# Performance work log

Measured on AMD Instinct MI355X. Metric: run time of the kernel, lower is better.

Reference implementation:

```python
import jax, jax.numpy as jnp
import numpy as np

COST_CLASS = 1.0
COST_OBJECTNESS = 5.0
COST_GIOU = 2.0
COST_CENTER = 10.0

B, Q, G, C = 32, 1024, 64, 256


def _lsa(cost):
    """Exact rectangular linear sum assignment (Jonker-Volgenant shortest
    augmenting path, same algorithm as scipy.optimize.linear_sum_assignment).
    cost: (R, Cc) float64 numpy array. Returns (row_ind, col_ind), row_ind sorted."""
    transposed = cost.shape[0] > cost.shape[1]
    if transposed:
        cost = cost.T
    n, m = cost.shape
    u = np.zeros(n)
    v = np.zeros(m)
    col4row = np.full(n, -1, dtype=np.int64)
    row4col = np.full(m, -1, dtype=np.int64)
    for cur_row in range(n):
        shortest = np.full(m, np.inf)
        path = np.full(m, -1, dtype=np.int64)
        SC = np.zeros(m, dtype=bool)
        SR_rows = []
        min_val = 0.0
        i = cur_row
        sink = -1
        while sink == -1:
            SR_rows.append(i)
            idx = np.where(~SC)[0]
            r = min_val + cost[i, idx] - u[i] - v[idx]
            better = r < shortest[idx]
            upd = idx[better]
            shortest[upd] = r[better]
            path[upd] = i
            j = idx[np.argmin(shortest[idx])]
            min_val = shortest[j]
            SC[j] = True
            if row4col[j] == -1:
                sink = j
            else:
                i = row4col[j]
        # dual variable update
        u[cur_row] += min_val
        for irow in SR_rows:
            if irow != cur_row:
                u[irow] += min_val - shortest[col4row[irow]]
        v[SC] -= min_val - shortest[SC]
        # augment along the alternating path back to cur_row
        j = sink
        while True:
            i = path[j]
            row4col[j] = i
            col4row[i], j = j, col4row[i]
            if i == cur_row:
                break
    if transposed:
        order = np.argsort(col4row)
        return col4row[order], np.arange(n)[order]
    return np.arange(n), col4row


def setup_inputs() -> dict:
    key = jax.random.key(0)
    k1, k2, k3, k4, k5 = jax.random.split(key, 5)
    return {
        "sem_cls_prob": jax.random.uniform(k1, (B, Q, C), dtype=jnp.float32),
        "objectness_prob": jax.random.uniform(k2, (B, Q), dtype=jnp.float32),
        "center_dist": jax.random.uniform(k3, (B, Q, G), dtype=jnp.float32),
        "gious": jax.random.uniform(k4, (B, Q, G), dtype=jnp.float32),
        "nactual_gt": jax.random.randint(k5, (B,), 0, G, dtype=jnp.int64)
        if jax.config.jax_enable_x64 else jax.random.randint(k5, (B,), 0, G).astype(jnp.int32),
    }


def reference(sem_cls_prob, objectness_prob, center_dist, gious, nactual_gt):
    batchsize, nprop = objectness_prob.shape
    # class_mat == 0 in the original module
    final_cost = (COST_OBJECTNESS * (-objectness_prob[..., None])
                  + COST_CENTER * center_dist
                  + COST_GIOU * (-gious))  # [B, Q, G]
    cost_np = np.asarray(final_cost, dtype=np.float64)
    ngt = np.asarray(nactual_gt)
    per_prop_gt_inds = np.zeros((batchsize, nprop), dtype=np.int64)
    proposal_matched_mask = np.zeros((batchsize, nprop), dtype=np.float32)
    for b in range(batchsize):  # per-batch independent Hungarian (as in source)
        g = int(ngt[b])
        if g > 0:
            rows, cols = _lsa(cost_np[b, :, :g])
            per_prop_gt_inds[b, rows] = cols
            proposal_matched_mask[b, rows] = 1.0
    return jnp.asarray(per_prop_gt_inds), jnp.asarray(proposal_matched_mask)
```

## Files before the change

kernel.cpp:

```cpp
#include <hip/hip_runtime.h>
#include <math.h>

#define B_ 32
#define Q_ 1024
#define G_ 64
#define K16 16

typedef double v16d __attribute__((ext_vector_type(16)));
typedef float  v16f __attribute__((ext_vector_type(16)));
typedef int    v16i __attribute__((ext_vector_type(16)));

#define REP16(OP) OP(0,0) OP(1,1) OP(2,2) OP(3,3) OP(4,4) OP(5,5) OP(6,6) OP(7,7) \
                  OP(8,8) OP(9,9) OP(10,a) OP(11,b) OP(12,c) OP(13,d) OP(14,e) OP(15,f)
#define REP16A(OP,A) OP(A,0,0) OP(A,1,1) OP(A,2,2) OP(A,3,3) OP(A,4,4) OP(A,5,5) OP(A,6,6) OP(A,7,7) \
                     OP(A,8,8) OP(A,9,9) OP(A,10,a) OP(A,11,b) OP(A,12,c) OP(A,13,d) OP(A,14,e) OP(A,15,f)

#define ROR1 0x121
#define ROR2 0x122
#define ROR4 0x124
#define ROR8 0x128
#define BC15 0x142
#define BC31 0x143

template<int CTRL>
__device__ __forceinline__ double dpp_f64(double x) {
    union { double d; int i[2]; } a; a.d = x;
    union { int i[2]; double d; } r;
    r.i[0] = __builtin_amdgcn_update_dpp(a.i[0], a.i[0], CTRL, 0xF, 0xF, false);
    r.i[1] = __builtin_amdgcn_update_dpp(a.i[1], a.i[1], CTRL, 0xF, 0xF, false);
    return r.d;
}
template<int CTRL>
__device__ __forceinline__ int dpp_i32(int x) {
    return __builtin_amdgcn_update_dpp(x, x, CTRL, 0xF, 0xF, false);
}

__device__ __forceinline__ double readlane_f64(double x, int sl) {
    const int s = __builtin_amdgcn_readfirstlane(sl);
    union { double d; int i2[2]; } a; a.d = x;
    union { int i2[2]; double d; } r;
    r.i2[0] = __builtin_amdgcn_readlane(a.i2[0], s);
    r.i2[1] = __builtin_amdgcn_readlane(a.i2[1], s);
    return r.d;
}
__device__ __forceinline__ double readlane_f64c(double x, int sl) {
    union { double d; int i2[2]; } a; a.d = x;
    union { int i2[2]; double d; } r;
    r.i2[0] = __builtin_amdgcn_readlane(a.i2[0], sl);
    r.i2[1] = __builtin_amdgcn_readlane(a.i2[1], sl);
    return r.d;
}
__device__ __forceinline__ float readlane_f32u(float x, int sl) {
    union { float f; int i; } a; a.f = x;
    union { int i; float f; } r;
    r.i = __builtin_amdgcn_readlane(a.i, __builtin_amdgcn_readfirstlane(sl));
    return r.f;
}
__device__ __forceinline__ int readlane_i32(int x, int sl) {
    return __builtin_amdgcn_readlane(x, __builtin_amdgcn_readfirstlane(sl));
}
__device__ __forceinline__ int readlane_i32c(int x, int sl) {
    return __builtin_amdgcn_readlane(x, sl);
}

__device__ __forceinline__ int sel16v_i(v16i p, int s) {
    const int t0_0 = (s & 1) ? p.s1 : p.s0;
    const int t0_1 = (s & 1) ? p.s3 : p.s2;
    const int t0_2 = (s & 1) ? p.s5 : p.s4;
    const int t0_3 = (s & 1) ? p.s7 : p.s6;
    const int t0_4 = (s & 1) ? p.s9 : p.s8;
    const int t0_5 = (s & 1) ? p.sb : p.sa;
    const int t0_6 = (s & 1) ? p.sd : p.sc;
    const int t0_7 = (s & 1) ? p.sf : p.se;
    const int t1_0 = (s & 2) ? t0_1 : t0_0;
    const int t1_1 = (s & 2) ? t0_3 : t0_2;
    const int t1_2 = (s & 2) ? t0_5 : t0_4;
    const int t1_3 = (s & 2) ? t0_7 : t0_6;
    const int a0 = (s & 4) ? t1_1 : t1_0;
    const int a1 = (s & 4) ? t1_3 : t1_2;
    return (s & 8) ? a1 : a0;
}
__device__ __forceinline__ double sel16v_d(v16d p, int s) {
    const double t0_0 = (s & 1) ? p.s1 : p.s0;
    const double t0_1 = (s & 1) ? p.s3 : p.s2;
    const double t0_2 = (s & 1) ? p.s5 : p.s4;
    const double t0_3 = (s & 1) ? p.s7 : p.s6;
    const double t0_4 = (s & 1) ? p.s9 : p.s8;
    const double t0_5 = (s & 1) ? p.sb : p.sa;
    const double t0_6 = (s & 1) ? p.sd : p.sc;
    const double t0_7 = (s & 1) ? p.sf : p.se;
    const double t1_0 = (s & 2) ? t0_1 : t0_0;
    const double t1_1 = (s & 2) ? t0_3 : t0_2;
    const double t1_2 = (s & 2) ? t0_5 : t0_4;
    const double t1_3 = (s & 2) ? t0_7 : t0_6;
    const double a0 = (s & 4) ? t1_1 : t1_0;
    const double a1 = (s & 4) ? t1_3 : t1_2;
    return (s & 8) ? a1 : a0;
}

__device__ __forceinline__ void lexpair(v16d c, int l,
                                        double& gv_o, int& jm_o) {
    const double a0 = fmin(c.s0, c.s1), a1 = fmin(c.s2, c.s3),
                 a2 = fmin(c.s4, c.s5), a3 = fmin(c.s6, c.s7),
                 a4 = fmin(c.s8, c.s9), a5 = fmin(c.sa, c.sb),
                 a6 = fmin(c.sc, c.sd), a7 = fmin(c.se, c.sf);
    const double b0 = fmin(a0, a1), b1 = fmin(a2, a3),
                 b2 = fmin(a4, a5), b3 = fmin(a6, a7);
    const double d0 = fmin(b0, b1), d1 = fmin(b2, b3);
    const double vloc = fmin(d0, d1);
    double v = vloc;
#define VS_(C) { const double pv = dpp_f64<C>(v); v = fmin(pv, v); }
    VS_(ROR1) VS_(ROR2) VS_(ROR4) VS_(ROR8) VS_(BC15) VS_(BC31)
#undef VS_
    const double gv = readlane_f64c(v, 63);
    const int bit3 = (d0 == gv) ? 0 : 1;
    const double bsel = bit3 ? b2 : b0;
    const int bit2 = (bsel == gv) ? 0 : 1;
    const double asel = bit2 ? (bit3 ? a6 : a2) : (bit3 ? a4 : a0);
    const int bit1 = (asel == gv) ? 0 : 1;
    const double csel = bit1 ? (bit2 ? (bit3 ? c.se : c.s6) : (bit3 ? c.sa : c.s2))
                             : (bit2 ? (bit3 ? c.sc : c.s4) : (bit3 ? c.s8 : c.s0));
    const int bit0 = (csel == gv) ? 0 : 1;
    const int kloc = (bit3 << 3) | (bit2 << 2) | (bit1 << 1) | bit0;
    int key = (vloc == gv) ? ((kloc << 6) | l) : 0x7FFFFFFF;
#define KS_(C) { const int pk = dpp_i32<C>(key); key = (pk < key) ? pk : key; }
    KS_(ROR1) KS_(ROR2) KS_(ROR4) KS_(ROR8) KS_(BC15) KS_(BC31)
#undef KS_
    jm_o = readlane_i32c(key, 63);
    gv_o = gv;
}

__global__ __launch_bounds__(256) void build_kernel(
    const float* __restrict__ obj, const float* __restrict__ cd,
    const float* __restrict__ gi, float* __restrict__ ct,
    float* __restrict__ pv, int* __restrict__ pj,
    float* __restrict__ pv2, int* __restrict__ pj2)
{
    __shared__ float tile[64][65];
    const int b  = blockIdx.y;
    const int jb = blockIdx.x << 6;
    const int t  = threadIdx.x;
    const float* objb = obj + (b << 10);
    const float4* cd4 = (const float4*)(cd + ((size_t)b << 16));
    const float4* gi4 = (const float4*)(gi + ((size_t)b << 16));

    #pragma unroll
    for (int p = 0; p < 4; ++p) {
        const int f  = t + (p << 8);
        const int jj = f >> 4;
        const int q  = f & 15;
        const int i0 = q << 2;
        const int j  = jb + jj;
        const float om = __fmul_rn(5.0f, -objb[j]);
        const float4 c4 = cd4[(j << 4) + q];
        const float4 q4 = gi4[(j << 4) + q];
        tile[i0 + 0][jj] = __fadd_rn(__fadd_rn(om, __fmul_rn(10.0f, c4.x)), __fmul_rn(2.0f, -q4.x));
        tile[i0 + 1][jj] = __fadd_rn(__fadd_rn(om, __fmul_rn(10.0f, c4.y)), __fmul_rn(2.0f, -q4.y));
        tile[i0 + 2][jj] = __fadd_rn(__fadd_rn(om, __fmul_rn(10.0f, c4.z)), __fmul_rn(2.0f, -q4.z));
        tile[i0 + 3][jj] = __fadd_rn(__fadd_rn(om, __fmul_rn(10.0f, c4.w)), __fmul_rn(2.0f, -q4.w));
    }
    __syncthreads();
    #pragma unroll
    for (int r = 0; r < 16; ++r) {
        const int idx = (r << 8) + t;
        const int i = idx >> 6, j2 = idx & 63;
        ct[(((size_t)(b << 6) + i) << 10) + jb + j2] = tile[i][j2];
    }
    if (t < 64) {
        float bv = tile[t][0]; int bc = 0;
        float sv = 1e30f;      int sc2 = 0;
        #pragma unroll 8
        for (int c = 1; c < 64; ++c) {
            const float v = tile[t][c];
            const bool t1 = v < bv;
            const bool t2 = (!t1) && (v < sv);
            sv  = t1 ? bv : (t2 ? v : sv);
            sc2 = t1 ? bc : (t2 ? c : sc2);
            bv  = t1 ? v : bv;
            bc  = t1 ? c : bc;
        }
        const int o = (((b << 6) + t) << 4) + blockIdx.x;
        pv[o]  = bv;  pj[o]  = jb + bc;
        pv2[o] = sv;  pj2[o] = jb + sc2;
    }
}

#define LD_W_(D,K,H) D.s##H = rp_[(K) << 6];
#define LD_N_(D,K,H) { const int idx_ = ((l + ((K) << 6)) << 6) + ri_; \
    D.s##H = __fadd_rn(__fadd_rn(objm.s##H, __fmul_rn(10.0f, cdb[idx_])), \
                       __fmul_rn(2.0f, -gib[idx_])); }
#define LOAD_ROW(ri, dst) { const int ri_ = (ri); \
    if (HASWS) { const float* rp_ = ctb + ((size_t)ri_ << 10) + l; REP16A(LD_W_, dst) } \
    else       { REP16A(LD_N_, dst) } }

template<bool HASWS>
__global__ __launch_bounds__(64, 1) void matcher_k(
    const float* __restrict__ obj, const float* __restrict__ cd,
    const float* __restrict__ gi, const int* __restrict__ ngt,
    const float* __restrict__ ct, const float* __restrict__ pv,
    const int* __restrict__ pj, const float* __restrict__ pv2,
    const int* __restrict__ pj2, float* __restrict__ out_ind,
    float* __restrict__ out_mask)
{
    const int b = blockIdx.x;
    const int l = threadIdx.x;
    const int g = ngt[b];

    const float* objb = obj + (b << 10);
    const float* cdb  = cd + ((size_t)b << 16);
    const float* gib  = gi + ((size_t)b << 16);
    const float* ctb  = HASWS ? (ct + ((size_t)(b << 6) << 10)) : (const float*)nullptr;

    v16f objm;
    if (!HASWS) {
#define OBJI_(K,H) objm.s##H = __fmul_rn(5.0f, -objb[l + (K << 6)]);
        REP16(OBJI_)
#undef OBJI_
    }

    float pre_v = 0.0f, sec_v = 0.0f; int pre_j = 0, sec_j = 0;
    if (HASWS) {
        const int base = ((b << 6) + l) << 4;
        const float4* pvq = (const float4*)(pv  + base);
        const int4*   pjq = (const int4*)(pj  + base);
        const float4* svq = (const float4*)(pv2 + base);
        const int4*   sjq = (const int4*)(pj2 + base);
        const float4 pA = pvq[0], pB = pvq[1], pC = pvq[2], pD = pvq[3];
        const int4   jA = pjq[0], jB = pjq[1], jC = pjq[2], jD = pjq[3];
        const float4 sA = svq[0], sB = svq[1], sC = svq[2], sD = svq[3];
        const int4   tA = sjq[0], tB = sjq[1], tC = sjq[2], tD = sjq[3];
        float bv = pA.x; int bj = jA.x; float sv = sA.x; int sj = tA.x;
#define MERGE_(CV,CJ,C2V,C2J) { const bool nb = (CV) < bv; \
    const bool s1 = (C2V) < bv; const bool s2 = (CV) < sv; \
    const float nsv = nb ? (s1 ? (C2V) : bv) : (s2 ? (CV) : sv); \
    const int   nsj = nb ? (s1 ? (C2J) : bj) : (s2 ? (CJ) : sj); \
    bj = nb ? (CJ) : bj; bv = nb ? (CV) : bv; sv = nsv; sj = nsj; }
        MERGE_(pA.y,jA.y,sA.y,tA.y) MERGE_(pA.z,jA.z,sA.z,tA.z) MERGE_(pA.w,jA.w,sA.w,tA.w)
        MERGE_(pB.x,jB.x,sB.x,tB.x) MERGE_(pB.y,jB.y,sB.y,tB.y) MERGE_(pB.z,jB.z,sB.z,tB.z) MERGE_(pB.w,jB.w,sB.w,tB.w)
        MERGE_(pC.x,jC.x,sC.x,tC.x) MERGE_(pC.y,jC.y,sC.y,tC.y) MERGE_(pC.z,jC.z,sC.z,tC.z) MERGE_(pC.w,jC.w,sC.w,tC.w)
        MERGE_(pD.x,jD.x,sD.x,tD.x) MERGE_(pD.y,jD.y,sD.y,tD.y) MERGE_(pD.z,jD.z,sD.z,tD.z) MERGE_(pD.w,jD.w,sD.w,tD.w)
#undef MERGE_
        pre_v = bv; pre_j = bj; sec_v = sv; sec_j = sj;
    } else if (g > 0) {
        for (int i = 0; i < g; ++i) {
            v16f c; LOAD_ROW(i, c)
            v16d c64;
#define CV_(K,H) c64.s##H = (double)c.s##H;
            REP16(CV_)
#undef CV_
            double gv; int j0;
            lexpair(c64, l, gv, j0);
            pre_v = (l == i) ? (float)gv : pre_v;
            pre_j = (l == i) ? j0 : pre_j;
        }
        sec_v = pre_v; sec_j = pre_j;
    }

    const double INF = __builtin_inf();
    double u_rep = 0.0;
    double m_rec = 0.0;
    bool   inSR  = false;
    int    c4r_rep = -1;
    unsigned asg   = 0u;
    unsigned dirty = 0u;
    v16d v_r, sh_r;
    v16i path;
    v16f c_cur, c_i;
#define INI_(K,H) { v_r.s##H = 0.0; sh_r.s##H = 0.0; path.s##H = 0; }
    REP16(INI_)
#undef INI_

    for (int cur = 0; cur < g; ++cur) {
        const float pre_vc = readlane_f32u(pre_v, cur);
        int jm = readlane_i32(pre_j, cur);
        double minv = (double)pre_vc;
        bool have_cur = false;
        {
            const int ow1 = jm & 63, sl1 = jm >> 6;
            const unsigned d1 = (unsigned)readlane_i32((int)dirty, ow1);
            if ((d1 >> sl1) & 1u) {
                const float sv_c = readlane_f32u(sec_v, cur);
                const int   sj_c = readlane_i32(sec_j, cur);
                const unsigned d2 = (unsigned)readlane_i32((int)dirty, sj_c & 63);
                if (!((d2 >> (sj_c >> 6)) & 1u)) {
                    const double vpj = readlane_f64(sel16v_d(v_r, sl1), ow1);
                    const double vA = (double)pre_vc - vpj;
                    const double vB = (double)sv_c;
                    const bool t = (vB < vA) || ((vB == vA) && (sj_c < jm));
                    minv = t ? vB : vA;
                    jm   = t ? sj_c : jm;
                } else {
                    LOAD_ROW(cur, c_cur) have_cur = true;
                    v16d rr0;
#define RR0_(K,H) rr0.s##H = (double)c_cur.s##H - v_r.s##H;
                    REP16(RR0_)
#undef RR0_
                    lexpair(rr0, l, minv, jm);
                }
            }
        }
        const unsigned long long mk0 = __ballot(c4r_rep == jm);

        if (mk0 == 0ull) {
            u_rep   = (l == cur) ? u_rep + minv : u_rep;
            c4r_rep = (l == cur) ? jm           : c4r_rep;
            asg     = (l == (jm & 63)) ? (asg | (1u << (jm >> 6))) : asg;
        } else {
            if (!have_cur) LOAD_ROW(cur, c_cur)
            int i = (int)__builtin_ctzll(mk0);
            LOAD_ROW(i, c_i)
            double ui = readlane_f64(u_rep, i);
            unsigned sc = (l == (jm & 63)) ? (1u << (jm >> 6)) : 0u;
            inSR  = (l == i);
            m_rec = minv;
#define SH0_(K,H) { sh_r.s##H = (double)c_cur.s##H - v_r.s##H; path.s##H = cur; }
            REP16(SH0_)
#undef SH0_

            int sink = -1;
            while (sink < 0) {
                v16d cand;
#define DST_(K,H) { const double rr = ((minv + (double)c_i.s##H) - ui) - v_r.s##H; \
                    const bool notSC = !((sc >> K) & 1u); \
                    const bool upd = notSC && (rr < sh_r.s##H);  \
                    sh_r.s##H = upd ? rr : sh_r.s##H; \
                    path.s##H = upd ? i : path.s##H; \
                    cand.s##H = notSC ? sh_r.s##H : INF; }
                REP16(DST_)
#undef DST_
                lexpair(cand, l, minv, jm);
                const unsigned long long mk = __ballot(c4r_rep == jm);
                if (l == (jm & 63)) sc |= (1u << (jm >> 6));
                if (mk == 0ull) {
                    sink = jm;
                } else {
                    i = (int)__builtin_ctzll(mk);
                    LOAD_ROW(i, c_i)
                    if (l == i) { inSR = true; m_rec = minv; }
                    ui = readlane_f64(u_rep, i);
                }
            }

            if (l == cur)       u_rep += minv;
            else if (inSR)      u_rep += minv - m_rec;
            unsigned chg = 0u;
#define VUP_(K,H) { const bool in_sc = (sc >> K) & 1u; \
                    const double nv = v_r.s##H - (minv - sh_r.s##H); \
                    chg = (in_sc && (sh_r.s##H != minv)) ? (chg | (1u << K)) : chg; \
                    v_r.s##H = in_sc ? nv : v_r.s##H; }
            REP16(VUP_)
#undef VUP_
            dirty |= chg;

            int j = sink;
            while (true) {
                const int so = j & 63, ss = j >> 6;
                const int ii = readlane_i32(sel16v_i(path, ss), so);
                const int nj = readlane_i32(c4r_rep, ii);
                asg     = (l == so) ? (asg | (1u << ss)) : asg;
                c4r_rep = (l == ii) ? j : c4r_rep;
                j = nj;
                if (ii == cur) break;
            }
        }
    }

#define OUT_(K,H) { const int jj = l + (K << 6); const bool a_ = (asg >> K) & 1u; \
    out_mask[(b << 10) + jj] = a_ ? 1.0f : 0.0f; \
    if (!a_) out_ind[(b << 10) + jj] = 0.0f; }
    REP16(OUT_)
#undef OUT_
    if (c4r_rep >= 0) out_ind[(b << 10) + c4r_rep] = (float)l;
}

extern "C" void kernel_launch(void* const* d_in, const int* in_sizes, int n_in,
                              void* d_out, int out_size, void* d_ws, size_t ws_size,
                              hipStream_t stream)
{
    const float* obj = (const float*)d_in[1];
    const float* cd  = (const float*)d_in[2];
    const float* gi  = (const float*)d_in[3];
    const int*   ngt = (const int*)d_in[4];
    float* out0 = (float*)d_out;
    float* out1 = out0 + B_ * Q_;

    const size_t ct_b = (size_t)B_ * G_ * Q_ * sizeof(float);
    const size_t pv_b = (size_t)B_ * G_ * 16 * sizeof(float);
    if (ws_size >= ct_b + 4 * pv_b) {
        float* ct  = (float*)d_ws;
        float* pv  = (float*)((char*)d_ws + ct_b);
        int*   pj  = (int*)  ((char*)d_ws + ct_b + pv_b);
        float* pv2 = (float*)((char*)d_ws + ct_b + 2 * pv_b);
        int*   pj2 = (int*)  ((char*)d_ws + ct_b + 3 * pv_b);
        build_kernel<<<dim3(16, B_), 256, 0, stream>>>(obj, cd, gi, ct, pv, pj, pv2, pj2);
        matcher_k<true><<<B_, 64, 0, stream>>>(obj, cd, gi, ngt, ct, pv, pj, pv2, pj2,
                                               out0, out1);
    } else {
        matcher_k<false><<<B_, 64, 0, stream>>>(obj, cd, gi, ngt, nullptr, nullptr,
                                                nullptr, nullptr, nullptr, out0, out1);
    }
}
```

Before: 160.2 us.

## Fuse cost-matrix build and Hungarian matcher into one per-batch kernel

Merges the separate build kernel (512 blocks) and the matcher kernel into a single kernel with one 256-thread block per batch. That block builds all 16 column tiles of the transposed cost matrix sequentially, keeps running best/second-best values in registers, and then runs the matcher on one wavefront. This removes a kernel launch and the pv/pj workspace round trip. In exchange, the build phase now runs on only 32 blocks instead of 512, so much less memory parallelism is available. It also adds a guard that skips the shortcut when the second-best column equals the best one.

```diff
diff --git a/kernel.cpp b/kernel.cpp
--- a/kernel.cpp
+++ b/kernel.cpp
@@ -130,132 +130,12 @@
     gv_o = gv;
 }
 
-__global__ __launch_bounds__(256) void build_kernel(
-    const float* __restrict__ obj, const float* __restrict__ cd,
-    const float* __restrict__ gi, float* __restrict__ ct,
-    float* __restrict__ pv, int* __restrict__ pj,
-    float* __restrict__ pv2, int* __restrict__ pj2)
+template<class LR>
+__device__ __forceinline__ void matcher_core(
+    const int l, const int g, LR load_row,
+    const float pre_v, const int pre_j, const float sec_v, const int sec_j,
+    float* __restrict__ out_ind_b, float* __restrict__ out_mask_b)
 {
-    __shared__ float tile[64][65];
-    const int b  = blockIdx.y;
-    const int jb = blockIdx.x << 6;
-    const int t  = threadIdx.x;
-    const float* objb = obj + (b << 10);
-    const float4* cd4 = (const float4*)(cd + ((size_t)b << 16));
-    const float4* gi4 = (const float4*)(gi + ((size_t)b << 16));
-
-    #pragma unroll
-    for (int p = 0; p < 4; ++p) {
-        const int f  = t + (p << 8);
-        const int jj = f >> 4;
-        const int q  = f & 15;
-        const int i0 = q << 2;
-        const int j  = jb + jj;
-        const float om = __fmul_rn(5.0f, -objb[j]);
-        const float4 c4 = cd4[(j << 4) + q];
-        const float4 q4 = gi4[(j << 4) + q];
-        tile[i0 + 0][jj] = __fadd_rn(__fadd_rn(om, __fmul_rn(10.0f, c4.x)), __fmul_rn(2.0f, -q4.x));
-        tile[i0 + 1][jj] = __fadd_rn(__fadd_rn(om, __fmul_rn(10.0f, c4.y)), __fmul_rn(2.0f, -q4.y));
-        tile[i0 + 2][jj] = __fadd_rn(__fadd_rn(om, __fmul_rn(10.0f, c4.z)), __fmul_rn(2.0f, -q4.z));
-        tile[i0 + 3][jj] = __fadd_rn(__fadd_rn(om, __fmul_rn(10.0f, c4.w)), __fmul_rn(2.0f, -q4.w));
-    }
-    __syncthreads();
-    #pragma unroll
-    for (int r = 0; r < 16; ++r) {
-        const int idx = (r << 8) + t;
-        const int i = idx >> 6, j2 = idx & 63;
-        ct[(((size_t)(b << 6) + i) << 10) + jb + j2] = tile[i][j2];
-    }
-    if (t < 64) {
-        float bv = tile[t][0]; int bc = 0;
-        float sv = 1e30f;      int sc2 = 0;
-        #pragma unroll 8
-        for (int c = 1; c < 64; ++c) {
-            const float v = tile[t][c];
-            const bool t1 = v < bv;
-            const bool t2 = (!t1) && (v < sv);
-            sv  = t1 ? bv : (t2 ? v : sv);
-            sc2 = t1 ? bc : (t2 ? c : sc2);
-            bv  = t1 ? v : bv;
-            bc  = t1 ? c : bc;
-        }
-        const int o = (((b << 6) + t) << 4) + blockIdx.x;
-        pv[o]  = bv;  pj[o]  = jb + bc;
-        pv2[o] = sv;  pj2[o] = jb + sc2;
-    }
-}
-
-#define LD_W_(D,K,H) D.s##H = rp_[(K) << 6];
-#define LD_N_(D,K,H) { const int idx_ = ((l + ((K) << 6)) << 6) + ri_; \
-    D.s##H = __fadd_rn(__fadd_rn(objm.s##H, __fmul_rn(10.0f, cdb[idx_])), \
-                       __fmul_rn(2.0f, -gib[idx_])); }
-#define LOAD_ROW(ri, dst) { const int ri_ = (ri); \
-    if (HASWS) { const float* rp_ = ctb + ((size_t)ri_ << 10) + l; REP16A(LD_W_, dst) } \
-    else       { REP16A(LD_N_, dst) } }
-
-template<bool HASWS>
-__global__ __launch_bounds__(64, 1) void matcher_k(
-    const float* __restrict__ obj, const float* __restrict__ cd,
-    const float* __restrict__ gi, const int* __restrict__ ngt,
-    const float* __restrict__ ct, const float* __restrict__ pv,
-    const int* __restrict__ pj, const float* __restrict__ pv2,
-    const int* __restrict__ pj2, float* __restrict__ out_ind,
-    float* __restrict__ out_mask)
-{
-    const int b = blockIdx.x;
-    const int l = threadIdx.x;
-    const int g = ngt[b];
-
-    const float* objb = obj + (b << 10);
-    const float* cdb  = cd + ((size_t)b << 16);
-    const float* gib  = gi + ((size_t)b << 16);
-    const float* ctb  = HASWS ? (ct + ((size_t)(b << 6) << 10)) : (const float*)nullptr;
-
-    v16f objm;
-    if (!HASWS) {
-#define OBJI_(K,H) objm.s##H = __fmul_rn(5.0f, -objb[l + (K << 6)]);
-        REP16(OBJI_)
-#undef OBJI_
-    }
-
-    float pre_v = 0.0f, sec_v = 0.0f; int pre_j = 0, sec_j = 0;
-    if (HASWS) {
-        const int base = ((b << 6) + l) << 4;
-        const float4* pvq = (const float4*)(pv  + base);
-        const int4*   pjq = (const int4*)(pj  + base);
-        const float4* svq = (const float4*)(pv2 + base);
-        const int4*   sjq = (const int4*)(pj2 + base);
-        const float4 pA = pvq[0], pB = pvq[1], pC = pvq[2], pD = pvq[3];
-        const int4   jA = pjq[0], jB = pjq[1], jC = pjq[2], jD = pjq[3];
-        const float4 sA = svq[0], sB = svq[1], sC = svq[2], sD = svq[3];
-        const int4   tA = sjq[0], tB = sjq[1], tC = sjq[2], tD = sjq[3];
-        float bv = pA.x; int bj = jA.x; float sv = sA.x; int sj = tA.x;
-#define MERGE_(CV,CJ,C2V,C2J) { const bool nb = (CV) < bv; \
-    const bool s1 = (C2V) < bv; const bool s2 = (CV) < sv; \
-    const float nsv = nb ? (s1 ? (C2V) : bv) : (s2 ? (CV) : sv); \
-    const int   nsj = nb ? (s1 ? (C2J) : bj) : (s2 ? (CJ) : sj); \
-    bj = nb ? (CJ) : bj; bv = nb ? (CV) : bv; sv = nsv; sj = nsj; }
-        MERGE_(pA.y,jA.y,sA.y,tA.y) MERGE_(pA.z,jA.z,sA.z,tA.z) MERGE_(pA.w,jA.w,sA.w,tA.w)
-        MERGE_(pB.x,jB.x,sB.x,tB.x) MERGE_(pB.y,jB.y,sB.y,tB.y) MERGE_(pB.z,jB.z,sB.z,tB.z) MERGE_(pB.w,jB.w,sB.w,tB.w)
-        MERGE_(pC.x,jC.x,sC.x,tC.x) MERGE_(pC.y,jC.y,sC.y,tC.y) MERGE_(pC.z,jC.z,sC.z,tC.z) MERGE_(pC.w,jC.w,sC.w,tC.w)
-        MERGE_(pD.x,jD.x,sD.x,tD.x) MERGE_(pD.y,jD.y,sD.y,tD.y) MERGE_(pD.z,jD.z,sD.z,tD.z) MERGE_(pD.w,jD.w,sD.w,tD.w)
-#undef MERGE_
-        pre_v = bv; pre_j = bj; sec_v = sv; sec_j = sj;
-    } else if (g > 0) {
-        for (int i = 0; i < g; ++i) {
-            v16f c; LOAD_ROW(i, c)
-            v16d c64;
-#define CV_(K,H) c64.s##H = (double)c.s##H;
-            REP16(CV_)
-#undef CV_
-            double gv; int j0;
-            lexpair(c64, l, gv, j0);
-            pre_v = (l == i) ? (float)gv : pre_v;
-            pre_j = (l == i) ? j0 : pre_j;
-        }
-        sec_v = pre_v; sec_j = pre_j;
-    }
-
     const double INF = __builtin_inf();
     double u_rep = 0.0;
     double m_rec = 0.0;
@@ -269,6 +149,9 @@
 #define INI_(K,H) { v_r.s##H = 0.0; sh_r.s##H = 0.0; path.s##H = 0; }
     REP16(INI_)
 #undef INI_
+#define Z16_(K,H) { c_cur.s##H = 0.0f; c_i.s##H = 0.0f; }
+    REP16(Z16_)
+#undef Z16_
 
     for (int cur = 0; cur < g; ++cur) {
         const float pre_vc = readlane_f32u(pre_v, cur);
@@ -282,15 +165,15 @@
                 const float sv_c = readlane_f32u(sec_v, cur);
                 const int   sj_c = readlane_i32(sec_j, cur);
                 const unsigned d2 = (unsigned)readlane_i32((int)dirty, sj_c & 63);
-                if (!((d2 >> (sj_c >> 6)) & 1u)) {
+                if (!((d2 >> (sj_c >> 6)) & 1u) && (sj_c != jm)) {
                     const double vpj = readlane_f64(sel16v_d(v_r, sl1), ow1);
                     const double vA = (double)pre_vc - vpj;
                     const double vB = (double)sv_c;
-                    const bool t = (vB < vA) || ((vB == vA) && (sj_c < jm));
-                    minv = t ? vB : vA;
-                    jm   = t ? sj_c : jm;
+                    const bool tt = (vB < vA) || ((vB == vA) && (sj_c < jm));
+                    minv = tt ? vB : vA;
+                    jm   = tt ? sj_c : jm;
                 } else {
-                    LOAD_ROW(cur, c_cur) have_cur = true;
+                    c_cur = load_row(cur); have_cur = true;
                     v16d rr0;
 #define RR0_(K,H) rr0.s##H = (double)c_cur.s##H - v_r.s##H;
                     REP16(RR0_)
@@ -306,9 +189,9 @@
             c4r_rep = (l == cur) ? jm           : c4r_rep;
             asg     = (l == (jm & 63)) ? (asg | (1u << (jm >> 6))) : asg;
         } else {
-            if (!have_cur) LOAD_ROW(cur, c_cur)
+            if (!have_cur) c_cur = load_row(cur);
             int i = (int)__builtin_ctzll(mk0);
-            LOAD_ROW(i, c_i)
+            c_i = load_row(i);
             double ui = readlane_f64(u_rep, i);
             unsigned sc = (l == (jm & 63)) ? (1u << (jm >> 6)) : 0u;
             inSR  = (l == i);
@@ -335,7 +218,7 @@
                     sink = jm;
                 } else {
                     i = (int)__builtin_ctzll(mk);
-                    LOAD_ROW(i, c_i)
+                    c_i = load_row(i);
                     if (l == i) { inSR = true; m_rec = minv; }
                     ui = readlane_f64(u_rep, i);
                 }
@@ -366,11 +249,134 @@
     }
 
 #define OUT_(K,H) { const int jj = l + (K << 6); const bool a_ = (asg >> K) & 1u; \
-    out_mask[(b << 10) + jj] = a_ ? 1.0f : 0.0f; \
-    if (!a_) out_ind[(b << 10) + jj] = 0.0f; }
+    out_mask_b[jj] = a_ ? 1.0f : 0.0f; \
+    if (!a_) out_ind_b[jj] = 0.0f; }
     REP16(OUT_)
 #undef OUT_
-    if (c4r_rep >= 0) out_ind[(b << 10) + c4r_rep] = (float)l;
+    if (c4r_rep >= 0) out_ind_b[c4r_rep] = (float)l;
+}
+
+__global__ __launch_bounds__(256, 1) void fused_k(
+    const float* __restrict__ obj, const float* __restrict__ cd,
+    const float* __restrict__ gi, const int* __restrict__ ngt,
+    float* __restrict__ ct, float* __restrict__ out_ind,
+    float* __restrict__ out_mask)
+{
+    __shared__ float tile[64][65];
+    const int b = blockIdx.x;
+    const int t = threadIdx.x;
+    const int g = ngt[b];
+    const float* objb = obj + (b << 10);
+    const float4* cd4 = (const float4*)(cd + ((size_t)b << 16));
+    const float4* gi4 = (const float4*)(gi + ((size_t)b << 16));
+    float* ctb = ct + ((size_t)(b << 6) << 10);
+
+    float rbv = __builtin_inff(), rsv = __builtin_inff();
+    int   rbj = 0, rsj = 0;
+
+    for (int cb = 0; cb < 16; ++cb) {
+        const int jb = cb << 6;
+        __syncthreads();
+        #pragma unroll
+        for (int p = 0; p < 4; ++p) {
+            const int f  = t + (p << 8);
+            const int jj = f >> 4;
+            const int q  = f & 15;
+            const int i0 = q << 2;
+            const int j  = jb + jj;
+            const float om = __fmul_rn(5.0f, -objb[j]);
+            const float4 c4 = cd4[(j << 4) + q];
+            const float4 q4 = gi4[(j << 4) + q];
+            tile[i0 + 0][jj] = __fadd_rn(__fadd_rn(om, __fmul_rn(10.0f, c4.x)), __fmul_rn(2.0f, -q4.x));
+            tile[i0 + 1][jj] = __fadd_rn(__fadd_rn(om, __fmul_rn(10.0f, c4.y)), __fmul_rn(2.0f, -q4.y));
+            tile[i0 + 2][jj] = __fadd_rn(__fadd_rn(om, __fmul_rn(10.0f, c4.z)), __fmul_rn(2.0f, -q4.z));
+            tile[i0 + 3][jj] = __fadd_rn(__fadd_rn(om, __fmul_rn(10.0f, c4.w)), __fmul_rn(2.0f, -q4.w));
+        }
+        __syncthreads();
+        #pragma unroll
+        for (int r = 0; r < 16; ++r) {
+            const int idx = (r << 8) + t;
+            const int i = idx >> 6, j2 = idx & 63;
+            ctb[((size_t)i << 10) + jb + j2] = tile[i][j2];
+        }
+        if (t < 64) {
+            float bv = tile[t][0]; int bc = 0;
+            float sv = 1e30f;      int sc2 = 0;
+            #pragma unroll 8
+            for (int c = 1; c < 64; ++c) {
+                const float v = tile[t][c];
+                const bool t1 = v < bv;
+                const bool t2 = (!t1) && (v < sv);
+                sv  = t1 ? bv : (t2 ? v : sv);
+                sc2 = t1 ? bc : (t2 ? c : sc2);
+                bv  = t1 ? v : bv;
+                bc  = t1 ? c : bc;
+            }
+            const float cv = bv, c2v = sv;
+            const int   cj = jb + bc, c2j = jb + sc2;
+            const bool nb = cv < rbv;
+            const bool s1 = c2v < rbv;
+            const bool s2 = cv < rsv;
+            const float nsv = nb ? (s1 ? c2v : rbv) : (s2 ? cv : rsv);
+            const int   nsj = nb ? (s1 ? c2j : rbj) : (s2 ? cj : rsj);
+            rbj = nb ? cj : rbj; rbv = nb ? cv : rbv; rsv = nsv; rsj = nsj;
+        }
+    }
+    __syncthreads();
+    if (t >= 64) return;
+
+    const int l = t;
+    auto load_row = [&](int ri) -> v16f {
+        v16f d; const float* rp_ = ctb + ((size_t)ri << 10) + l;
+#define LDW_(D,K,H) D.s##H = rp_[(K) << 6];
+        REP16A(LDW_, d)
+#undef LDW_
+        return d;
+    };
+    matcher_core(l, g, load_row, rbv, rbj, rsv, rsj,
+                 out_ind + (b << 10), out_mask + (b << 10));
+}
+
+__global__ __launch_bounds__(64, 1) void matcher_nws(
+    const float* __restrict__ obj, const float* __restrict__ cd,
+    const float* __restrict__ gi, const int* __restrict__ ngt,
+    float* __restrict__ out_ind, float* __restrict__ out_mask)
+{
+    const int b = blockIdx.x;
+    const int l = threadIdx.x;
+    const int g = ngt[b];
+    const float* objb = obj + (b << 10);
+    const float* cdb  = cd + ((size_t)b << 16);
+    const float* gib  = gi + ((size_t)b << 16);
+
+    v16f objm;
+#define OBJI_(K,H) objm.s##H = __fmul_rn(5.0f, -objb[l + (K << 6)]);
+    REP16(OBJI_)
+#undef OBJI_
+    auto load_row = [&](int ri) -> v16f {
+        v16f d;
+#define LDN_(D,K,H) { const int idx_ = ((l + ((K) << 6)) << 6) + ri; \
+    D.s##H = __fadd_rn(__fadd_rn(objm.s##H, __fmul_rn(10.0f, cdb[idx_])), \
+                       __fmul_rn(2.0f, -gib[idx_])); }
+        REP16A(LDN_, d)
+#undef LDN_
+        return d;
+    };
+
+    float pre_v = 0.0f; int pre_j = 0;
+    for (int i = 0; i < g; ++i) {
+        v16f c = load_row(i);
+        v16d c64;
+#define CV_(K,H) c64.s##H = (double)c.s##H;
+        REP16(CV_)
+#undef CV_
+        double gv; int j0;
+        lexpair(c64, l, gv, j0);
+        pre_v = (l == i) ? (float)gv : pre_v;
+        pre_j = (l == i) ? j0 : pre_j;
+    }
+    matcher_core(l, g, load_row, pre_v, pre_j, pre_v, pre_j,
+                 out_ind + (b << 10), out_mask + (b << 10));
 }
 
 extern "C" void kernel_launch(void* const* d_in, const int* in_sizes, int n_in,
@@ -385,18 +391,10 @@
     float* out1 = out0 + B_ * Q_;
 
     const size_t ct_b = (size_t)B_ * G_ * Q_ * sizeof(float);
-    const size_t pv_b = (size_t)B_ * G_ * 16 * sizeof(float);
-    if (ws_size >= ct_b + 4 * pv_b) {
-        float* ct  = (float*)d_ws;
-        float* pv  = (float*)((char*)d_ws + ct_b);
-        int*   pj  = (int*)  ((char*)d_ws + ct_b + pv_b);
-        float* pv2 = (float*)((char*)d_ws + ct_b + 2 * pv_b);
-        int*   pj2 = (int*)  ((char*)d_ws + ct_b + 3 * pv_b);
-        build_kernel<<<dim3(16, B_), 256, 0, stream>>>(obj, cd, gi, ct, pv, pj, pv2, pj2);
-        matcher_k<true><<<B_, 64, 0, stream>>>(obj, cd, gi, ngt, ct, pv, pj, pv2, pj2,
-                                               out0, out1);
+    if (ws_size >= ct_b) {
+        float* ct = (float*)d_ws;
+        fused_k<<<B_, 256, 0, stream>>>(obj, cd, gi, ngt, ct, out0, out1);
     } else {
-        matcher_k<false><<<B_, 64, 0, stream>>>(obj, cd, gi, ngt, nullptr, nullptr,
-                                                nullptr, nullptr, nullptr, out0, out1);
+        matcher_nws<<<B_, 64, 0, stream>>>(obj, cd, gi, ngt, out0, out1);
     }
 }
```

Result: slower. 199.3 us (+24.5%).
